# Optimization experiments

Measured on AMD Instinct MI355X. Metric: run time of the kernel, lower is better.

## Reference

```python
import jax, jax.numpy as jnp
import numpy as np

B, S = 256, 512
PAD = 64          # padded tail per slate
QN = 256          # query_num (one query per batch row)
PADDED_Y_VALUE = -1.0
EPS = 1e-10       # DEFAULT_EPS
ETA = 0.01
ETA1 = 0.01       # self.eta1 is undefined in the source (bug); we use eta
TAU1, TAU2 = 1e-3, 1e-4
GAMMA_V, GAMMA_R = 0.1, 0.1
TOPK = 10
SIG_ALPHA = 2.0
C_SIG = 2.0
LN2 = 0.6931471805599453


def setup_inputs() -> dict:
    key = jax.random.key(0)
    ks = jax.random.split(key, 10)
    y_pred = jax.random.normal(ks[0], (B, S), jnp.float32)
    y_true = jax.random.uniform(ks[1], (B, S), jnp.float32) * 4.0
    y_true = y_true.at[:, S - PAD:].set(PADDED_Y_VALUE)   # padded docs
    qid = jnp.broadcast_to(jnp.arange(B, dtype=jnp.int32)[:, None], (B, S))
    indices = jnp.broadcast_to(jnp.arange(S, dtype=jnp.int32)[None, :], (B, S))
    num_pos = jax.random.randint(ks[2], (B,), 1, 32).astype(jnp.int32)
    num_item = jnp.full((B,), S - PAD, jnp.int32)
    ideal_dcg = jax.random.uniform(ks[3], (B,), jnp.float32) * 10.0 + 1.0
    u = jax.random.uniform(ks[4], (QN + 2, S + 2), jnp.float32)
    v = jax.random.uniform(ks[5], (QN + 2, S + 2), jnp.float32) * 0.1
    lambda_q = jax.random.uniform(ks[6], (QN + 2,), jnp.float32)
    z_q = jax.random.uniform(ks[7], (QN + 2,), jnp.float32) * 0.1
    r_q = jax.random.uniform(ks[8], (QN + 2,), jnp.float32) * 0.1
    s_q = jax.random.uniform(ks[9], (QN + 2,), jnp.float32) + 0.5
    return dict(y_pred=y_pred, y_true=y_true, qid=qid, indices=indices,
                num_pos=num_pos, num_item=num_item, ideal_dcg=ideal_dcg,
                u=u, v=v, lambda_q=lambda_q, z_q=z_q, r_q=r_q, s_q=s_q)


def _fwd(y_pred, y_true, qid, indices, num_pos, num_item, ideal_dcg,
         u, v, lambda_q, z_q, r_q, s_q):
    dt = y_pred.dtype
    pad = y_true == PADDED_Y_VALUE
    yp = jnp.where(pad, 0.0, y_pred)                 # padded scores zeroed (safe)
    fin = (~pad).astype(dt)
    n_fin = jnp.sum(fin, axis=-1)                    # num_of_noninf [B]
    # pairwise squared hinge: diffs[b,i,j] = yp[b,j] - yp[b,i]
    diffs = yp[:, None, :] - yp[:, :, None]          # [B,S,S]
    pair_mask = fin[:, None, :] * fin[:, :, None]
    hinge = jnp.maximum(diffs + 1.0, 0.0) ** 2
    g = jnp.sum(pair_mask * hinge, axis=-1) / n_fin[:, None] + EPS   # [B,S]
    idcg = ideal_dcg + EPS
    G = jnp.where(pad, 0.0, 2.0 ** jnp.maximum(y_true, 0.0) - 1.0)
    ni = num_item.astype(dt)[:, None]
    # moving-average u/v estimator update at (qid+1, indices+1)
    qf = qid.reshape(-1) + 1
    idf = indices.reshape(-1) + 1
    u_old = u[qf, idf]
    v_old = v[qf, idf]
    nabla_u_g = u_old - jax.lax.stop_gradient(g).reshape(-1)
    v_new = (1.0 - GAMMA_V) * v_old + GAMMA_V * nabla_u_g
    u_new = u_old - ETA1 * v_new
    g_u = u_new.reshape(g.shape)                     # read-back of updated u
    log2t = jnp.log2(2.0 + ni * g_u)
    nabla_f_g = G * ni / (log2t ** 2 * (2.0 + ni * g_u) * LN2)
    # top-k lambda machinery (uses PRE-update lambda_q / s_q, as in source)
    qb = qid[:, 0] + 1
    lam = lambda_q[qb]
    pld = jnp.where(pad, 0.0, jax.lax.stop_gradient(y_pred) - lam[:, None])
    sig1 = jax.nn.sigmoid(pld / TAU1)
    sig_a = jax.nn.sigmoid(pld * SIG_ALPHA)
    nabla_f_g = nabla_f_g * C_SIG * sig_a
    weight_1 = C_SIG * sig_a * (1.0 - sig_a)
    temp_term = sig1 * (1.0 - sig1) / TAU1
    L_hess = TAU2 + jnp.sum(fin * temp_term, axis=1) / n_fin       # [B]
    f_g_u = -G / log2t                                              # [B,S]
    # s_q moving-average update; the source is shape-inconsistent here
    # ([B]-shaped buffer vs [B,S] term) -- we reduce with a masked mean (see notes)
    nabla_s_phi = L_hess * s_q[qb] + jnp.sum(fin * (G / log2t), axis=-1) / n_fin
    r_new = (1.0 - GAMMA_R) * r_q[qb] + GAMMA_R * nabla_s_phi
    s_new = s_q[qb] - ETA1 * r_new
    hessian_term = jnp.sum(fin * temp_term * yp, axis=1) / n_fin / s_new  # [B]
    per_item = nabla_f_g * g + weight_1 * f_g_u * (yp - hessian_term[:, None])
    # faithful torch broadcasting: [B,1] * [B] -> [B,B], then global mean
    loss = jnp.mean(num_pos.astype(dt)[:, None]
                    * jnp.mean(per_item, axis=-1) / idcg[:, None])
    return loss


def reference(y_pred, y_true, qid, indices, num_pos, num_item, ideal_dcg,
              u, v, lambda_q, z_q, r_q, s_q):
    return _fwd(y_pred, y_true, qid, indices, num_pos, num_item, ideal_dcg,
                u, v, lambda_q, z_q, r_q, s_q)
```

## Files before the change

kernel.cpp:

```cpp
#include <hip/hip_runtime.h>
#include <math.h>

constexpr int BB  = 256;
constexpr int SS  = 512;
constexpr int SP2 = SS + 2;

__device__ __forceinline__ float2 block_red_sum_max(float v, float m,
                                                    volatile float* sm) {
    #pragma unroll
    for (int off = 32; off > 0; off >>= 1) {
        v += __shfl_down(v, off, 64);
        m  = fmaxf(m, __shfl_down(m, off, 64));
    }
    const int wid  = threadIdx.x >> 6;
    const int lane = threadIdx.x & 63;
    __syncthreads();
    if (lane == 0) { sm[wid] = v; sm[4 + wid] = m; }
    __syncthreads();
    return make_float2((sm[0] + sm[1]) + (sm[2] + sm[3]),
                       fmaxf(fmaxf(sm[4], sm[5]), fmaxf(sm[6], sm[7])));
}

__device__ __forceinline__ float3 block_red3(float a, float b, float c,
                                             volatile float* sm) {
    #pragma unroll
    for (int off = 32; off > 0; off >>= 1) {
        a += __shfl_down(a, off, 64);
        b += __shfl_down(b, off, 64);
        c += __shfl_down(c, off, 64);
    }
    const int wid  = threadIdx.x >> 6;
    const int lane = threadIdx.x & 63;
    __syncthreads();
    if (lane == 0) { sm[wid] = a; sm[4 + wid] = b; sm[8 + wid] = c; }
    __syncthreads();
    return make_float3((sm[0] + sm[1]) + (sm[2] + sm[3]),
                       (sm[4] + sm[5]) + (sm[6] + sm[7]),
                       (sm[8] + sm[9]) + (sm[10] + sm[11]));
}

__device__ __forceinline__ float sigmoidf_(float x) {
    return 1.0f / (1.0f + expf(-x));
}

__global__ __launch_bounds__(256)
void ndcg_row_kernel(const float* __restrict__ y_pred,
                     const float* __restrict__ y_true,
                     const int*   __restrict__ qid,
                     const int*   __restrict__ indices,
                     const int*   __restrict__ num_pos,
                     const int*   __restrict__ num_item,
                     const float* __restrict__ ideal_dcg,
                     const float* __restrict__ u_buf,
                     const float* __restrict__ v_buf,
                     const float* __restrict__ lambda_q,
                     const float* __restrict__ r_q,
                     const float* __restrict__ s_q,
                     float2* __restrict__ ws) {
    __shared__ float sh_ys[SS] __attribute__((aligned(16)));
    __shared__ float sm[12];

    const int b = blockIdx.x;
    const int t = threadIdx.x;

    const float2 yt2 = *(const float2*)&y_true[b * SS + 2 * t];
    const float2 yp2 = *(const float2*)&y_pred[b * SS + 2 * t];
    const int2   qd2 = *(const int2*)  &qid[b * SS + 2 * t];
    const int2   ix2 = *(const int2*)  &indices[b * SS + 2 * t];

    const bool  fi0 = (yt2.x != -1.0f), fi1 = (yt2.y != -1.0f);
    const float f0  = fi0 ? 1.0f : 0.0f, f1 = fi1 ? 1.0f : 0.0f;
    float2 zs;
    zs.x = fi0 ? yp2.x : -1.0e4f;
    zs.y = fi1 ? yp2.y : -1.0e4f;
    *(float2*)&sh_ys[2 * t] = zs;
    const float G0 = fi0 ? (exp2f(fmaxf(yt2.x, 0.0f)) - 1.0f) : 0.0f;
    const float G1 = fi1 ? (exp2f(fmaxf(yt2.y, 0.0f)) - 1.0f) : 0.0f;

    const int   ui0 = (qd2.x + 1) * SP2 + (ix2.x + 1);
    const int   ui1 = (qd2.y + 1) * SP2 + (ix2.y + 1);
    const float u_old0 = u_buf[ui0], v_old0 = v_buf[ui0];
    const float u_old1 = u_buf[ui1], v_old1 = v_buf[ui1];
    const int   qb  = qid[b * SS] + 1;
    const float lam = lambda_q[qb];
    const float ni  = (float)num_item[b];
    const float sqv = s_q[qb];

    __syncthreads();

    const float mI = fi1 ? (float)(2 * t + 1) : (fi0 ? (float)(2 * t) : -1.0f);
    const float2 nm = block_red_sum_max(f0 + f1, mI, sm);
    const float n_fin = nm.x;
    const int   jmax  = (int)nm.y;
    const int   j4cnt = (jmax + 4) >> 2;

    const float yi1_0 = 1.0f - f0 * yp2.x;
    const float yi1_1 = 1.0f - f1 * yp2.y;
    const float4* ys4 = (const float4*)sh_ys;
    float a00 = 0.f, a01 = 0.f, a02 = 0.f, a03 = 0.f;
    float a10 = 0.f, a11 = 0.f, a12 = 0.f, a13 = 0.f;
    #pragma unroll 4
    for (int j = 0; j < j4cnt; ++j) {
        const float4 y = ys4[j];
        float h;
        h = fmaxf(y.x + yi1_0, 0.0f); a00 = fmaf(h, h, a00);
        h = fmaxf(y.y + yi1_0, 0.0f); a01 = fmaf(h, h, a01);
        h = fmaxf(y.z + yi1_0, 0.0f); a02 = fmaf(h, h, a02);
        h = fmaxf(y.w + yi1_0, 0.0f); a03 = fmaf(h, h, a03);
        h = fmaxf(y.x + yi1_1, 0.0f); a10 = fmaf(h, h, a10);
        h = fmaxf(y.y + yi1_1, 0.0f); a11 = fmaf(h, h, a11);
        h = fmaxf(y.z + yi1_1, 0.0f); a12 = fmaf(h, h, a12);
        h = fmaxf(y.w + yi1_1, 0.0f); a13 = fmaf(h, h, a13);
    }
    const float inv_nfin = 1.0f / n_fin;
    float g[2];
    g[0] = f0 * (((a00 + a01) + (a02 + a03)) * inv_nfin) + 1e-10f;
    g[1] = f1 * (((a10 + a11) + (a12 + a13)) * inv_nfin) + 1e-10f;

    const float uo[2] = {u_old0, u_old1}, vo[2] = {v_old0, v_old1};
    const float fn[2] = {f0, f1}, Gk[2] = {G0, G1};
    const float yv[2] = {yp2.x, yp2.y};
    float Shess = 0.f, Sphi = 0.f, Shy = 0.f, P1 = 0.f, P2 = 0.f, P3 = 0.f;
    #pragma unroll
    for (int k = 0; k < 2; ++k) {
        const float nug   = uo[k] - g[k];
        const float v_new = 0.9f * vo[k] + 0.1f * nug;
        const float g_u   = uo[k] - 0.01f * v_new;
        const float t2    = fmaf(ni, g_u, 2.0f);
        const float l2t   = log2f(t2);
        const float rl2t  = 1.0f / l2t;

        float nfg = Gk[k] * ni / (l2t * l2t * t2 * 0.6931471805599453f);

        const float pld  = (fn[k] != 0.0f) ? (yv[k] - lam) : 0.0f;
        const float sig1 = sigmoidf_(pld * 1000.0f);
        const float siga = sigmoidf_(pld * 2.0f);
        nfg *= 2.0f * siga;
        const float w1  = 2.0f * siga * (1.0f - siga);
        const float tt  = sig1 * (1.0f - sig1) * 1000.0f;
        const float fgu = -Gk[k] * rl2t;
        const float ypz = fn[k] * yv[k];

        Shess += fn[k] * tt;
        Sphi  += fn[k] * (Gk[k] * rl2t);
        Shy   += fn[k] * tt * ypz;
        P1  = fmaf(nfg, g[k], P1);
        P2 += w1 * fgu * ypz;
        P3 += w1 * fgu;
    }
    const float3 rA = block_red3(Shess, Sphi, Shy, sm);
    const float3 rB = block_red3(P1,    P2,   P3,  sm);

    if (t == 0) {
        const float L_hess  = 1e-4f + rA.x * inv_nfin;
        const float nsp     = L_hess * sqv + rA.y * inv_nfin;
        const float r_new   = 0.9f * r_q[qb] + 0.1f * nsp;
        const float s_new   = sqv - 0.01f * r_new;
        const float hess    = (rA.z * inv_nfin) / s_new;
        const float row_sum = rB.x + rB.y - hess * rB.z;
        ws[b] = make_float2(row_sum * (1.0f / (float)SS),
                            (float)num_pos[b] / (ideal_dcg[b] + 1e-10f));
    }
}

__global__ __launch_bounds__(64)
void ndcg_final_kernel(const float2* __restrict__ ws, float* __restrict__ out) {
    const int t = threadIdx.x;
    float r = 0.f, a = 0.f;
    #pragma unroll
    for (int k = 0; k < 4; ++k) {
        const float2 p = ws[t + 64 * k];
        r += p.x; a += p.y;
    }
    #pragma unroll
    for (int off = 32; off > 0; off >>= 1) {
        r += __shfl_down(r, off, 64);
        a += __shfl_down(a, off, 64);
    }
    if (t == 0)
        out[0] = (a * (1.0f / (float)BB)) * (r * (1.0f / (float)BB));
}

extern "C" void kernel_launch(void* const* d_in, const int* in_sizes, int n_in,
                              void* d_out, int out_size, void* d_ws, size_t ws_size,
                              hipStream_t stream) {
    const float* y_pred    = (const float*)d_in[0];
    const float* y_true    = (const float*)d_in[1];
    const int*   qid       = (const int*)  d_in[2];
    const int*   indices   = (const int*)  d_in[3];
    const int*   num_pos   = (const int*)  d_in[4];
    const int*   num_item  = (const int*)  d_in[5];
    const float* ideal_dcg = (const float*)d_in[6];
    const float* u_buf     = (const float*)d_in[7];
    const float* v_buf     = (const float*)d_in[8];
    const float* lambda_q  = (const float*)d_in[9];
    const float* r_q       = (const float*)d_in[11];
    const float* s_q       = (const float*)d_in[12];

    float2* ws = (float2*)d_ws;

    ndcg_row_kernel<<<BB, 256, 0, stream>>>(y_pred, y_true, qid, indices,
                                            num_pos, num_item, ideal_dcg,
                                            u_buf, v_buf, lambda_q, r_q, s_q, ws);
    ndcg_final_kernel<<<1, 64, 0, stream>>>(ws, (float*)d_out);
}
```

Baseline: 16.98 us.

## Fuse final reduction into row kernel via last-block atomic counter; pack hinge math

Drops the second launch. Each block publishes its partial row result with atomic stores and bumps a global counter, and the block that finishes last performs the final 256-entry reduction inside the same kernel. The inner hinge loop is also rewritten with 2-wide float vectors so the compiler can emit packed FP32 add/max/fma. This relies on the counter never being reset: it uses the counter modulo 256 and assumes the workspace starts zeroed and keeps its value across calls. It also adds atomic traffic at the tail of each block.

New measurement: 18.23 us. +7.4%, slower.

```diff
diff --git a/kernel.cpp b/kernel.cpp
--- a/kernel.cpp
+++ b/kernel.cpp
@@ -4,6 +4,8 @@
 constexpr int BB  = 256;
 constexpr int SS  = 512;
 constexpr int SP2 = SS + 2;
+
+typedef float f32x2 __attribute__((ext_vector_type(2)));
 
 __device__ __forceinline__ float2 block_red_sum_max(float v, float m,
                                                     volatile float* sm) {
@@ -56,9 +58,12 @@
                      const float* __restrict__ lambda_q,
                      const float* __restrict__ r_q,
                      const float* __restrict__ s_q,
-                     float2* __restrict__ ws) {
+                     float2* __restrict__ ws,
+                     unsigned int* __restrict__ counter,
+                     float* __restrict__ out) {
     __shared__ float sh_ys[SS] __attribute__((aligned(16)));
     __shared__ float sm[12];
+    __shared__ int   lastSh;
 
     const int b = blockIdx.x;
     const int t = threadIdx.x;
@@ -94,28 +99,26 @@
     const int   jmax  = (int)nm.y;
     const int   j4cnt = (jmax + 4) >> 2;
 
-    const float yi1_0 = 1.0f - f0 * yp2.x;
-    const float yi1_1 = 1.0f - f1 * yp2.y;
+    const f32x2 yb0 = (f32x2)(1.0f - f0 * yp2.x);
+    const f32x2 yb1 = (f32x2)(1.0f - f1 * yp2.y);
+    const f32x2 z2  = (f32x2)0.0f;
     const float4* ys4 = (const float4*)sh_ys;
-    float a00 = 0.f, a01 = 0.f, a02 = 0.f, a03 = 0.f;
-    float a10 = 0.f, a11 = 0.f, a12 = 0.f, a13 = 0.f;
+    f32x2 a00 = z2, a01 = z2, a10 = z2, a11 = z2;
     #pragma unroll 4
     for (int j = 0; j < j4cnt; ++j) {
         const float4 y = ys4[j];
-        float h;
-        h = fmaxf(y.x + yi1_0, 0.0f); a00 = fmaf(h, h, a00);
-        h = fmaxf(y.y + yi1_0, 0.0f); a01 = fmaf(h, h, a01);
-        h = fmaxf(y.z + yi1_0, 0.0f); a02 = fmaf(h, h, a02);
-        h = fmaxf(y.w + yi1_0, 0.0f); a03 = fmaf(h, h, a03);
-        h = fmaxf(y.x + yi1_1, 0.0f); a10 = fmaf(h, h, a10);
-        h = fmaxf(y.y + yi1_1, 0.0f); a11 = fmaf(h, h, a11);
-        h = fmaxf(y.z + yi1_1, 0.0f); a12 = fmaf(h, h, a12);
-        h = fmaxf(y.w + yi1_1, 0.0f); a13 = fmaf(h, h, a13);
+        const f32x2 lo = {y.x, y.y};
+        const f32x2 hi = {y.z, y.w};
+        f32x2 d;
+        d = __builtin_elementwise_max(lo + yb0, z2); a00 = __builtin_elementwise_fma(d, d, a00);
+        d = __builtin_elementwise_max(hi + yb0, z2); a01 = __builtin_elementwise_fma(d, d, a01);
+        d = __builtin_elementwise_max(lo + yb1, z2); a10 = __builtin_elementwise_fma(d, d, a10);
+        d = __builtin_elementwise_max(hi + yb1, z2); a11 = __builtin_elementwise_fma(d, d, a11);
     }
     const float inv_nfin = 1.0f / n_fin;
     float g[2];
-    g[0] = f0 * (((a00 + a01) + (a02 + a03)) * inv_nfin) + 1e-10f;
-    g[1] = f1 * (((a10 + a11) + (a12 + a13)) * inv_nfin) + 1e-10f;
+    g[0] = f0 * (((a00.x + a00.y) + (a01.x + a01.y)) * inv_nfin) + 1e-10f;
+    g[1] = f1 * (((a10.x + a10.y) + (a11.x + a11.y)) * inv_nfin) + 1e-10f;
 
     const float uo[2] = {u_old0, u_old1}, vo[2] = {v_old0, v_old1};
     const float fn[2] = {f0, f1}, Gk[2] = {G0, G1};
@@ -158,27 +161,33 @@
         const float s_new   = sqv - 0.01f * r_new;
         const float hess    = (rA.z * inv_nfin) / s_new;
         const float row_sum = rB.x + rB.y - hess * rB.z;
-        ws[b] = make_float2(row_sum * (1.0f / (float)SS),
-                            (float)num_pos[b] / (ideal_dcg[b] + 1e-10f));
-    }
-}
-
-__global__ __launch_bounds__(64)
-void ndcg_final_kernel(const float2* __restrict__ ws, float* __restrict__ out) {
-    const int t = threadIdx.x;
-    float r = 0.f, a = 0.f;
-    #pragma unroll
-    for (int k = 0; k < 4; ++k) {
-        const float2 p = ws[t + 64 * k];
-        r += p.x; a += p.y;
-    }
-    #pragma unroll
-    for (int off = 32; off > 0; off >>= 1) {
-        r += __shfl_down(r, off, 64);
-        a += __shfl_down(a, off, 64);
-    }
-    if (t == 0)
-        out[0] = (a * (1.0f / (float)BB)) * (r * (1.0f / (float)BB));
+        float* wf = (float*)&ws[b];
+        __hip_atomic_store(wf,     row_sum * (1.0f / (float)SS),
+                           __ATOMIC_RELAXED, __HIP_MEMORY_SCOPE_AGENT);
+        __hip_atomic_store(wf + 1, (float)num_pos[b] / (ideal_dcg[b] + 1e-10f),
+                           __ATOMIC_RELAXED, __HIP_MEMORY_SCOPE_AGENT);
+        const unsigned int old = __hip_atomic_fetch_add(counter, 1u,
+                           __ATOMIC_ACQ_REL, __HIP_MEMORY_SCOPE_AGENT);
+        lastSh = ((old & (BB - 1)) == (BB - 1)) ? 1 : 0;
+    }
+    __syncthreads();
+
+    if (lastSh && t < 64) {
+        float r = 0.f, a = 0.f;
+        #pragma unroll
+        for (int k = 0; k < 4; ++k) {
+            const float* p = (const float*)&ws[t + 64 * k];
+            r += __hip_atomic_load(p,     __ATOMIC_RELAXED, __HIP_MEMORY_SCOPE_AGENT);
+            a += __hip_atomic_load(p + 1, __ATOMIC_RELAXED, __HIP_MEMORY_SCOPE_AGENT);
+        }
+        #pragma unroll
+        for (int off = 32; off > 0; off >>= 1) {
+            r += __shfl_down(r, off, 64);
+            a += __shfl_down(a, off, 64);
+        }
+        if (t == 0)
+            out[0] = (a * (1.0f / (float)BB)) * (r * (1.0f / (float)BB));
+    }
 }
 
 extern "C" void kernel_launch(void* const* d_in, const int* in_sizes, int n_in,
@@ -197,10 +206,11 @@
     const float* r_q       = (const float*)d_in[11];
     const float* s_q       = (const float*)d_in[12];
 
-    float2* ws = (float2*)d_ws;
+    float2*       ws      = (float2*)d_ws;
+    unsigned int* counter = (unsigned int*)(ws + BB);
 
     ndcg_row_kernel<<<BB, 256, 0, stream>>>(y_pred, y_true, qid, indices,
                                             num_pos, num_item, ideal_dcg,
-                                            u_buf, v_buf, lambda_q, r_q, s_q, ws);
-    ndcg_final_kernel<<<1, 64, 0, stream>>>(ws, (float*)d_out);
-}
+                                            u_buf, v_buf, lambda_q, r_q, s_q,
+                                            ws, counter, (float*)d_out);
+}
```
